# Kernel tuning notes

Hardware: AMD Instinct MI355X
Metric: run time of the kernel (lower is better)

The kernel has to match this reference:

```python
import jax, jax.numpy as jnp
import numpy as np

N_HEAD = 16
N_FEAT = 1024
D_K = N_FEAT // N_HEAD
BATCH = 8
SEQ = 1024
LN_EPS = 1e-5
MIN_VAL = float(np.finfo(np.float32).min)


def setup_inputs() -> dict:
    key = jax.random.key(0)
    ks = jax.random.split(key, 8)
    s = 0.02  # small init scale for weights to keep activations sane
    return {
        "x": jax.random.normal(ks[0], (BATCH, SEQ, N_FEAT), jnp.float32),
        "pos_k": jax.random.normal(ks[1], (SEQ, SEQ, D_K), jnp.float32) * s,
        "mask": jnp.ones((BATCH, SEQ, SEQ), jnp.int32),
        "ln_scale": jnp.ones((N_FEAT,), jnp.float32),
        "ln_bias": jnp.zeros((N_FEAT,), jnp.float32),
        "wq": jax.random.normal(ks[2], (N_FEAT, N_FEAT), jnp.float32) * s,
        "bq": jnp.zeros((N_FEAT,), jnp.float32),
        "wk": jax.random.normal(ks[3], (N_FEAT, N_FEAT), jnp.float32) * s,
        "bk": jnp.zeros((N_FEAT,), jnp.float32),
        "wv": jax.random.normal(ks[4], (N_FEAT, N_FEAT), jnp.float32) * s,
        "bv": jnp.zeros((N_FEAT,), jnp.float32),
        "wo": jax.random.normal(ks[5], (N_FEAT, N_FEAT), jnp.float32) * s,
        "bo": jnp.zeros((N_FEAT,), jnp.float32),
    }


def reference(x, pos_k, mask, ln_scale, ln_bias, wq, bq, wk, bk, wv, bv, wo, bo):
    b, t, f = x.shape
    h, d = N_HEAD, D_K
    # LayerNorm over feature dim
    mu = jnp.mean(x, axis=-1, keepdims=True)
    var = jnp.mean((x - mu) ** 2, axis=-1, keepdims=True)
    xn = (x - mu) / jnp.sqrt(var + LN_EPS) * ln_scale + ln_bias
    # QKV projections (torch Linear: y = x @ W^T + b), split heads -> (b, h, t, d)
    q = (xn @ wq.T + bq).reshape(b, t, h, d).transpose(0, 2, 1, 3)
    k = (xn @ wk.T + bk).reshape(b, t, h, d).transpose(0, 2, 1, 3)
    v = (xn @ wv.T + bv).reshape(b, t, h, d).transpose(0, 2, 1, 3)
    # content score A and relative-position score B
    A = jnp.einsum("bhtd,bhsd->bhts", q, k)
    B = jnp.einsum("bhtd,tsd->bhts", q, pos_k)
    scores = (A + B) / jnp.sqrt(jnp.asarray(d, scores_dtype := x.dtype))
    m = (mask[:, None, :, :] == 0)  # (b, 1, t, s) broadcast over heads
    scores = jnp.where(m, MIN_VAL, scores)
    attn = jax.nn.softmax(scores, axis=-1)
    attn = jnp.where(m, 0.0, attn)
    out = jnp.einsum("bhts,bhsd->bhtd", attn, v)
    out = out.transpose(0, 2, 1, 3).reshape(b, t, h * d)
    return out @ wo.T + bo
```

## Files before the change

### kernel.cpp

```cpp
#include <hip/hip_runtime.h>
#include <hip/hip_bf16.h>

typedef unsigned short ushort_t;
typedef short short8 __attribute__((ext_vector_type(8)));
typedef unsigned short ushort8 __attribute__((ext_vector_type(8)));
typedef unsigned short ushortx4 __attribute__((ext_vector_type(4)));
typedef float fx4 __attribute__((ext_vector_type(4)));
typedef int ix4 __attribute__((ext_vector_type(4)));

#define MFMA(a, b, c) __builtin_amdgcn_mfma_f32_16x16x32_bf16((a), (b), (c), 0, 0, 0)

#define QSCALE 0.18033688011112042f

__device__ __forceinline__ ushort_t f2bf(float f) {
  __hip_bfloat16 h = __float2bfloat16(f);
  return *(ushort_t*)&h;
}
__device__ __forceinline__ float bf2f(ushort_t h) {
  union { unsigned u; float f; } c; c.u = ((unsigned)h) << 16;
  return c.f;
}
__device__ __forceinline__ void gload16(const ushort_t* g, ushort_t* l) {
  __builtin_amdgcn_global_load_lds((const __attribute__((address_space(1))) void*)g,
                                   (__attribute__((address_space(3))) void*)l, 16, 0, 0);
}
template <int R>
__device__ __forceinline__ float fp8sel(unsigned u) {
  return __builtin_amdgcn_cvt_f32_fp8((int)u, R);
}
__device__ __forceinline__ fx4 fp8x4(unsigned u) {
  fx4 r;
  r[0] = fp8sel<0>(u); r[1] = fp8sel<1>(u); r[2] = fp8sel<2>(u); r[3] = fp8sel<3>(u);
  return r;
}

__global__ __launch_bounds__(256) void cvt4_kernel(const float* __restrict__ s0,
                                                   const float* __restrict__ s1,
                                                   const float* __restrict__ s2,
                                                   const float* __restrict__ s3,
                                                   ushort_t* __restrict__ d0,
                                                   ushort_t* __restrict__ d1,
                                                   ushort_t* __restrict__ d2,
                                                   ushort_t* __restrict__ d3) {
  int bi = blockIdx.x;
  const float* src = (bi < 1024) ? s0 : (bi < 2048) ? s1 : (bi < 3072) ? s2 : s3;
  ushort_t* dst = (bi < 1024) ? d0 : (bi < 2048) ? d1 : (bi < 3072) ? d2 : d3;
  int i = (bi & 1023) * 256 + threadIdx.x;
  fx4 v = *(const fx4*)&src[(size_t)i * 4];
  ushortx4 o;
#pragma unroll
  for (int j = 0; j < 4; ++j) o[j] = f2bf(v[j]);
  *(ushortx4*)&dst[(size_t)i * 4] = o;
}

__global__ __launch_bounds__(256) void ln_kernel(const float* __restrict__ x,
                                                 const float* __restrict__ sc,
                                                 const float* __restrict__ bi,
                                                 ushort_t* __restrict__ xn) {
  __shared__ float red[8];
  int row = blockIdx.x, tid = threadIdx.x;
  const float* xr = x + (size_t)row * 1024;
  fx4 v = *(const fx4*)&xr[tid * 4];
  float s = v[0] + v[1] + v[2] + v[3];
  float s2 = v[0] * v[0] + v[1] * v[1] + v[2] * v[2] + v[3] * v[3];
#pragma unroll
  for (int m = 32; m >= 1; m >>= 1) {
    s += __shfl_xor(s, m);
    s2 += __shfl_xor(s2, m);
  }
  int wave = tid >> 6;
  if ((tid & 63) == 0) { red[wave * 2] = s; red[wave * 2 + 1] = s2; }
  __syncthreads();
  s = red[0] + red[2] + red[4] + red[6];
  s2 = red[1] + red[3] + red[5] + red[7];
  float mu = s * (1.f / 1024.f);
  float var = s2 * (1.f / 1024.f) - mu * mu;
  float rs = rsqrtf(var + 1e-5f);
  fx4 scv = *(const fx4*)&sc[tid * 4];
  fx4 biv = *(const fx4*)&bi[tid * 4];
  ushortx4 o;
#pragma unroll
  for (int j = 0; j < 4; ++j) o[j] = f2bf((v[j] - mu) * rs * scv[j] + biv[j]);
  *(ushortx4*)&xn[(size_t)row * 1024 + tid * 4] = o;
}

__global__ __launch_bounds__(256) void maskpack_kernel(const int* __restrict__ mask,
                                                       unsigned* __restrict__ bits) {
  __shared__ unsigned char nib[256];
  int row = blockIdx.x, tid = threadIdx.x;
  ix4 m = *(const ix4*)&mask[(size_t)row * 1024 + tid * 4];
  nib[tid] = (unsigned char)((m[0] != 0 ? 1 : 0) | (m[1] != 0 ? 2 : 0) |
                             (m[2] != 0 ? 4 : 0) | (m[3] != 0 ? 8 : 0));
  __syncthreads();
  if (tid < 32) {
    unsigned w = 0;
#pragma unroll
    for (int j = 0; j < 8; ++j) w |= ((unsigned)nib[tid * 8 + j]) << (j * 4);
    bits[(size_t)row * 32 + tid] = w;
  }
}

template <int F32OUT>
__global__ __launch_bounds__(256) void gemm_bt(const ushort_t* __restrict__ A,
                                               const ushort_t* __restrict__ B,
                                               const float* __restrict__ b0,
                                               const float* __restrict__ b1,
                                               const float* __restrict__ b2, void* C,
                                               int M, int N, int K, float os0, float os1) {
  __shared__ ushort_t lA[4096];
  __shared__ ushort_t lB[4096];
  int bm = blockIdx.y * 128, bn = blockIdx.x * 128;
  int tid = threadIdx.x;
  int wave = tid >> 6, lane = tid & 63;
  int wm = (wave >> 1) * 64, wn = (wave & 1) * 64;
  int l15 = lane & 15, lg = lane >> 4;
  int r0 = tid >> 2, c0 = (tid & 3) * 8;
  int g1 = 256 + tid, r1 = g1 >> 2, c1 = (g1 & 3) * 8;
  int lb0 = (wave * 64) * 8;
  int lb1 = (256 + wave * 64) * 8;
  fx4 acc[4][4] = {};
  for (int k0 = 0; k0 < K; k0 += 32) {
    __syncthreads();
    gload16(&A[(size_t)(bm + r0) * K + k0 + c0], &lA[lb0]);
    gload16(&A[(size_t)(bm + r1) * K + k0 + c1], &lA[lb1]);
    gload16(&B[(size_t)(bn + r0) * K + k0 + c0], &lB[lb0]);
    gload16(&B[(size_t)(bn + r1) * K + k0 + c1], &lB[lb1]);
    __syncthreads();
    short8 af[4], bf[4];
#pragma unroll
    for (int i = 0; i < 4; ++i) af[i] = *(const short8*)&lA[(wm + i * 16 + l15) * 32 + lg * 8];
#pragma unroll
    for (int i = 0; i < 4; ++i) bf[i] = *(const short8*)&lB[(wn + i * 16 + l15) * 32 + lg * 8];
#pragma unroll
    for (int i = 0; i < 4; ++i)
#pragma unroll
      for (int j = 0; j < 4; ++j) acc[i][j] = MFMA(af[i], bf[j], acc[i][j]);
  }
#pragma unroll
  for (int j = 0; j < 4; ++j) {
    int n = bn + wn + j * 16 + l15;
    const float* bp = (n < 1024) ? b0 : (n < 2048) ? b1 : b2;
    float bv = bp[n & 1023];
    float sc = (n < 1024) ? os0 : os1;
#pragma unroll
    for (int i = 0; i < 4; ++i) {
      int mr = bm + wm + i * 16 + lg * 4;
#pragma unroll
      for (int r = 0; r < 4; ++r) {
        float val = (acc[i][j][r] + bv) * sc;
        if (F32OUT)
          ((float*)C)[(size_t)(mr + r) * N + n] = val;
        else
          ((ushort_t*)C)[(size_t)(mr + r) * N + n] = f2bf(val);
      }
    }
  }
}

__device__ __forceinline__ void loadset(const float* base, int c, fx4* r) {
  const float* p = base + (size_t)c * 1024;
  r[0] = *(const fx4*)p;
  r[1] = *(const fx4*)(p + 4);
  r[2] = *(const fx4*)(p + 32);
  r[3] = *(const fx4*)(p + 36);
}
__device__ __forceinline__ void cvtset(const fx4* r, short8& f0, short8& f1) {
#pragma unroll
  for (int j = 0; j < 4; ++j) {
    f0[j] = (short)f2bf(r[0][j]); f0[j + 4] = (short)f2bf(r[1][j]);
    f1[j] = (short)f2bf(r[2][j]); f1[j + 4] = (short)f2bf(r[3][j]);
  }
}

__global__ __launch_bounds__(512, 4) void ball_kernel(const ushort_t* __restrict__ qkv,
                                                      const float* __restrict__ pos_k,
                                                      unsigned char* __restrict__ B8) {
  __shared__ ushort_t lq[128 * 64];
  int t = blockIdx.y, sx = blockIdx.x;
  int tid = threadIdx.x, wave = tid >> 6, lane = tid & 63, l15 = lane & 15, lg = lane >> 4;
  const float* pk = pos_k + (size_t)t * 65536;
  int sw = sx * 512 + wave * 64;
  const float* base = pk + (size_t)(sw + l15) * 64 + lg * 8;

  fx4 raw[4][4];
#pragma unroll
  for (int c = 0; c < 4; ++c) loadset(base, c, raw[c]);

#pragma unroll
  for (int it = 0; it < 2; ++it) {
    int u = tid + it * 512;
    int row = u >> 3, cu = u & 7;
    ushort8 vv = *(const ushort8*)&qkv[((size_t)((row >> 4) * 1024 + t)) * 3072 + (row & 15) * 64 + cu * 8];
    *(ushort8*)&lq[(row * 128 + ((cu * 16) ^ ((row & 7) << 4))) >> 1] = vv;
  }
  __syncthreads();

  short8 af0[4], af1[4];
#pragma unroll
  for (int c = 0; c < 4; ++c) cvtset(raw[c], af0[c], af1[c]);

#pragma unroll
  for (int j = 0; j < 8; ++j) {
    int row_ = j * 16 + l15;
    int cb_ = (row_ & 7) << 4;
    short8 q0 = *(const short8*)&lq[(row_ * 128 + ((lg * 16) ^ cb_)) >> 1];
    short8 q1 = *(const short8*)&lq[(row_ * 128 + ((64 + lg * 16) ^ cb_)) >> 1];
    fx4 z = {};
    size_t rb = ((size_t)row_ << 20) + (size_t)t * 1024 + (size_t)sw;
#pragma unroll
    for (int c = 0; c < 4; ++c) {
      fx4 a = MFMA(af0[c], q0, z);
      a = MFMA(af1[c], q1, a);
      int u = __builtin_amdgcn_cvt_pk_fp8_f32(a[0], a[1], 0, false);
      u = __builtin_amdgcn_cvt_pk_fp8_f32(a[2], a[3], u, true);
      *(unsigned*)&B8[rb + c * 16 + lg * 4] = (unsigned)u;
    }
  }
}

__global__ __launch_bounds__(256) void attn_kernel(const ushort_t* __restrict__ qkv,
                                                   const unsigned char* __restrict__ B8,
                                                   const unsigned* __restrict__ mbits,
                                                   ushort_t* __restrict__ out) {
  __shared__ ushort_t lK[64][72];
  __shared__ ushort_t lVt[64][72];
  __shared__ ushort_t lP[4][2][16][72];
  int bh = blockIdx.y, b = bh >> 4, h = bh & 15;
  int t0 = blockIdx.x * 128;
  int tid = threadIdx.x, wave = tid >> 6, lane = tid & 63, l15 = lane & 15, lg = lane >> 4;
  int twA = t0 + wave * 16, twB = twA + 64;
  short8 qfA[2], qfB[2];
#pragma unroll
  for (int ks = 0; ks < 2; ++ks) {
    qfA[ks] = *(const short8*)&qkv[((size_t)(b * 1024 + twA + l15)) * 3072 + h * 64 + ks * 32 + lg * 8];
    qfB[ks] = *(const short8*)&qkv[((size_t)(b * 1024 + twB + l15)) * 3072 + h * 64 + ks * 32 + lg * 8];
  }
  fx4 oA[4] = {}, oB[4] = {};
  float lsumA = 0.f, lsumB = 0.f;
  const unsigned* mrowA = &mbits[((size_t)b * 1024 + twA + l15) * 32];
  const unsigned* mrowB = &mbits[((size_t)b * 1024 + twB + l15) * 32];
  size_t ballA = ((size_t)bh * 1024 + twA + l15) * 1024;
  size_t ballB = ((size_t)bh * 1024 + twB + l15) * 1024;

  int rs = tid >> 3, c8g = tid & 7, c8 = c8g * 8;
  const ushort_t* kbase = &qkv[((size_t)(b * 1024) + rs) * 3072 + 1024 + h * 64 + c8];
  const ushort_t* vbase = &qkv[((size_t)(b * 1024) + rs) * 3072 + 2048 + h * 64 + c8];
  ushort8 kr0 = *(const ushort8*)(kbase);
  ushort8 kr1 = *(const ushort8*)(kbase + 32 * 3072);
  ushort8 vr0 = *(const ushort8*)(vbase);
  ushort8 vr1 = *(const ushort8*)(vbase + 32 * 3072);
  int vs0 = (rs + 8 * c8g) & 63;
  int vs1 = (rs + 32 + 8 * c8g) & 63;

  unsigned n8A[4], n8B[4];
#pragma unroll
  for (int mf = 0; mf < 4; ++mf) {
    n8A[mf] = *(const unsigned*)&B8[ballA + mf * 16 + lg * 4];
    n8B[mf] = *(const unsigned*)&B8[ballB + mf * 16 + lg * 4];
  }
  uint2 nmA = *(const uint2*)&mrowA[0];
  uint2 nmB = *(const uint2*)&mrowB[0];

  for (int s0 = 0; s0 < 1024; s0 += 64) {
    __syncthreads();
    *(ushort8*)&lK[rs][c8] = kr0;
    *(ushort8*)&lK[rs + 32][c8] = kr1;
#pragma unroll
    for (int j = 0; j < 8; ++j) {
      lVt[c8 + j][vs0] = vr0[j];
      lVt[c8 + j][vs1] = vr1[j];
    }
    __syncthreads();
    if (s0 + 64 < 1024) {
      size_t off = (size_t)(s0 + 64) * 3072;
      kr0 = *(const ushort8*)(kbase + off);
      kr1 = *(const ushort8*)(kbase + off + 32 * 3072);
      vr0 = *(const ushort8*)(vbase + off);
      vr1 = *(const ushort8*)(vbase + off + 32 * 3072);
    }
    __builtin_amdgcn_sched_barrier(0);
    unsigned long long wbA = ((unsigned long long)nmA.y << 32) | nmA.x;
    unsigned long long wbB = ((unsigned long long)nmB.y << 32) | nmB.x;
    float pA[16], pB[16];
#pragma unroll
    for (int mf = 0; mf < 4; ++mf) {
      short8 kf0 = *(const short8*)&lK[mf * 16 + l15][lg * 8];
      short8 kf1 = *(const short8*)&lK[mf * 16 + l15][32 + lg * 8];
      fx4 cA = {}, cB = {};
      cA = MFMA(kf0, qfA[0], cA);
      cA = MFMA(kf1, qfA[1], cA);
      cB = MFMA(kf0, qfB[0], cB);
      cB = MFMA(kf1, qfB[1], cB);
      fx4 dA = fp8x4(n8A[mf]);
      fx4 dB = fp8x4(n8B[mf]);
#pragma unroll
      for (int r = 0; r < 4; ++r) {
        pA[mf * 4 + r] = exp2f(cA[r] + dA[r]);
        pB[mf * 4 + r] = exp2f(cB[r] + dB[r]);
      }
    }
    if (!__all((wbA == ~0ull) && (wbB == ~0ull))) {
#pragma unroll
      for (int i = 0; i < 16; ++i) {
        int sl = (i >> 2) * 16 + lg * 4 + (i & 3);
        if (!((wbA >> sl) & 1ull)) pA[i] = 0.f;
        if (!((wbB >> sl) & 1ull)) pB[i] = 0.f;
      }
    }
    if (s0 + 64 < 1024) {
#pragma unroll
      for (int mf = 0; mf < 4; ++mf) {
        n8A[mf] = *(const unsigned*)&B8[ballA + s0 + 64 + mf * 16 + lg * 4];
        n8B[mf] = *(const unsigned*)&B8[ballB + s0 + 64 + mf * 16 + lg * 4];
      }
      nmA = *(const uint2*)&mrowA[(s0 + 64) >> 5];
      nmB = *(const uint2*)&mrowB[(s0 + 64) >> 5];
    }
    __builtin_amdgcn_sched_barrier(0);
    float psA = 0.f, psB = 0.f;
#pragma unroll
    for (int i = 0; i < 16; ++i) { psA += pA[i]; psB += pB[i]; }
    lsumA += psA;
    lsumB += psB;
#pragma unroll
    for (int mf = 0; mf < 4; ++mf) {
      ushortx4 pk4A, pk4B;
#pragma unroll
      for (int r = 0; r < 4; ++r) { pk4A[r] = f2bf(pA[mf * 4 + r]); pk4B[r] = f2bf(pB[mf * 4 + r]); }
      *(ushortx4*)&lP[wave][0][l15][mf * 16 + lg * 4] = pk4A;
      *(ushortx4*)&lP[wave][1][l15][mf * 16 + lg * 4] = pk4B;
    }
#pragma unroll
    for (int ks = 0; ks < 2; ++ks) {
      short8 pfA = *(const short8*)&lP[wave][0][l15][ks * 32 + lg * 8];
      short8 pfB = *(const short8*)&lP[wave][1][l15][ks * 32 + lg * 8];
#pragma unroll
      for (int nf = 0; nf < 4; ++nf) {
        int d_ = nf * 16 + l15;
        int sb_ = (ks * 32 + lg * 8 + 8 * (d_ >> 3)) & 63;
        short8 vf = *(const short8*)&lVt[d_][sb_];
        oA[nf] = MFMA(pfA, vf, oA[nf]);
        oB[nf] = MFMA(pfB, vf, oB[nf]);
      }
    }
  }
  lsumA += __shfl_xor(lsumA, 16);
  lsumA += __shfl_xor(lsumA, 32);
  lsumB += __shfl_xor(lsumB, 16);
  lsumB += __shfl_xor(lsumB, 32);
  float rlA = (lsumA > 0.f) ? 1.f / lsumA : 0.f;
  float rlB = (lsumB > 0.f) ? 1.f / lsumB : 0.f;
  float rwA[4], rwB[4];
#pragma unroll
  for (int r = 0; r < 4; ++r) {
    rwA[r] = __shfl(rlA, lg * 4 + r);
    rwB[r] = __shfl(rlB, lg * 4 + r);
  }
#pragma unroll
  for (int nf = 0; nf < 4; ++nf)
#pragma unroll
    for (int r = 0; r < 4; ++r) {
      out[((size_t)(b * 1024 + twA + lg * 4 + r)) * 1024 + h * 64 + nf * 16 + l15] =
          f2bf(oA[nf][r] * rwA[r]);
      out[((size_t)(b * 1024 + twB + lg * 4 + r)) * 1024 + h * 64 + nf * 16 + l15] =
          f2bf(oB[nf][r] * rwB[r]);
    }
}

extern "C" void kernel_launch(void* const* d_in, const int* in_sizes, int n_in, void* d_out,
                              int out_size, void* d_ws, size_t ws_size, hipStream_t stream) {
  (void)in_sizes; (void)n_in; (void)out_size; (void)ws_size;
  const float* x = (const float*)d_in[0];
  const float* pos_k = (const float*)d_in[1];
  const int* mask = (const int*)d_in[2];
  const float* ln_scale = (const float*)d_in[3];
  const float* ln_bias = (const float*)d_in[4];
  const float* wq = (const float*)d_in[5];
  const float* bq = (const float*)d_in[6];
  const float* wk = (const float*)d_in[7];
  const float* bk = (const float*)d_in[8];
  const float* wv = (const float*)d_in[9];
  const float* bv = (const float*)d_in[10];
  const float* wo = (const float*)d_in[11];
  const float* bo = (const float*)d_in[12];
  float* out = (float*)d_out;
  char* ws = (char*)d_ws;
  const size_t MB = 1ull << 20;
  ushort_t* xn = (ushort_t*)(ws + 0 * MB);
  ushort_t* qkv = (ushort_t*)(ws + 16 * MB);
  ushort_t* ao = (ushort_t*)(ws + 64 * MB);
  ushort_t* wqb = (ushort_t*)(ws + 80 * MB);
  ushort_t* wkb = (ushort_t*)(ws + 82 * MB);
  ushort_t* wvb = (ushort_t*)(ws + 84 * MB);
  ushort_t* wob = (ushort_t*)(ws + 86 * MB);
  unsigned char* ball8 = (unsigned char*)(ws + 88 * MB);
  unsigned* mbits = (unsigned*)(ws + 0 * MB);

  cvt4_kernel<<<4096, 256, 0, stream>>>(wq, wk, wv, wo, wqb, wkb, wvb, wob);
  ln_kernel<<<8192, 256, 0, stream>>>(x, ln_scale, ln_bias, xn);
  gemm_bt<0><<<dim3(24, 64), 256, 0, stream>>>(xn, wqb, bq, bk, bv, qkv, 8192, 3072, 1024,
                                               QSCALE, 1.f);
  maskpack_kernel<<<8192, 256, 0, stream>>>(mask, mbits);
  ball_kernel<<<dim3(2, 1024), 512, 0, stream>>>(qkv, pos_k, ball8);
  attn_kernel<<<dim3(8, 128), 256, 0, stream>>>(qkv, ball8, mbits, ao);
  gemm_bt<1><<<dim3(8, 64), 256, 0, stream>>>(ao, wob, bo, bo, bo, out, 8192, 1024, 1024,
                                              1.f, 1.f);
}
```

Measured before the change: 354.5 us.

## Merge prep kernels into one launch and double-buffer pos_k loads in ball kernel

The weight-conversion, LayerNorm and mask-packing kernels are combined into one prep kernel dispatched by block index, and the mask bits move to a separate workspace offset so they no longer alias xn. The ball kernel now has each block handle all 1024 s positions for one t. Each wave covers 128 columns in two halves and prefetches the second pos_k chunk while the first half's MFMAs run. This cuts launch count and hides pos_k load latency, but halves the ball grid and raises register pressure from the prefetch.

```diff
diff --git a/kernel.cpp b/kernel.cpp
--- a/kernel.cpp
+++ b/kernel.cpp
@@ -34,69 +34,69 @@
   return r;
 }
 
-__global__ __launch_bounds__(256) void cvt4_kernel(const float* __restrict__ s0,
-                                                   const float* __restrict__ s1,
-                                                   const float* __restrict__ s2,
-                                                   const float* __restrict__ s3,
-                                                   ushort_t* __restrict__ d0,
-                                                   ushort_t* __restrict__ d1,
-                                                   ushort_t* __restrict__ d2,
-                                                   ushort_t* __restrict__ d3) {
-  int bi = blockIdx.x;
-  const float* src = (bi < 1024) ? s0 : (bi < 2048) ? s1 : (bi < 3072) ? s2 : s3;
-  ushort_t* dst = (bi < 1024) ? d0 : (bi < 2048) ? d1 : (bi < 3072) ? d2 : d3;
-  int i = (bi & 1023) * 256 + threadIdx.x;
-  fx4 v = *(const fx4*)&src[(size_t)i * 4];
-  ushortx4 o;
-#pragma unroll
-  for (int j = 0; j < 4; ++j) o[j] = f2bf(v[j]);
-  *(ushortx4*)&dst[(size_t)i * 4] = o;
-}
-
-__global__ __launch_bounds__(256) void ln_kernel(const float* __restrict__ x,
-                                                 const float* __restrict__ sc,
-                                                 const float* __restrict__ bi,
-                                                 ushort_t* __restrict__ xn) {
+__global__ __launch_bounds__(256) void prep_kernel(const float* __restrict__ wq,
+                                                   const float* __restrict__ wk,
+                                                   const float* __restrict__ wv,
+                                                   const float* __restrict__ wo,
+                                                   ushort_t* __restrict__ wqb,
+                                                   ushort_t* __restrict__ wkb,
+                                                   ushort_t* __restrict__ wvb,
+                                                   ushort_t* __restrict__ wob,
+                                                   const float* __restrict__ x,
+                                                   const float* __restrict__ sc,
+                                                   const float* __restrict__ bi,
+                                                   ushort_t* __restrict__ xn,
+                                                   const int* __restrict__ mask,
+                                                   unsigned* __restrict__ bits) {
   __shared__ float red[8];
-  int row = blockIdx.x, tid = threadIdx.x;
-  const float* xr = x + (size_t)row * 1024;
-  fx4 v = *(const fx4*)&xr[tid * 4];
-  float s = v[0] + v[1] + v[2] + v[3];
-  float s2 = v[0] * v[0] + v[1] * v[1] + v[2] * v[2] + v[3] * v[3];
-#pragma unroll
-  for (int m = 32; m >= 1; m >>= 1) {
-    s += __shfl_xor(s, m);
-    s2 += __shfl_xor(s2, m);
-  }
-  int wave = tid >> 6;
-  if ((tid & 63) == 0) { red[wave * 2] = s; red[wave * 2 + 1] = s2; }
-  __syncthreads();
-  s = red[0] + red[2] + red[4] + red[6];
-  s2 = red[1] + red[3] + red[5] + red[7];
-  float mu = s * (1.f / 1024.f);
-  float var = s2 * (1.f / 1024.f) - mu * mu;
-  float rs = rsqrtf(var + 1e-5f);
-  fx4 scv = *(const fx4*)&sc[tid * 4];
-  fx4 biv = *(const fx4*)&bi[tid * 4];
-  ushortx4 o;
-#pragma unroll
-  for (int j = 0; j < 4; ++j) o[j] = f2bf((v[j] - mu) * rs * scv[j] + biv[j]);
-  *(ushortx4*)&xn[(size_t)row * 1024 + tid * 4] = o;
-}
-
-__global__ __launch_bounds__(256) void maskpack_kernel(const int* __restrict__ mask,
-                                                       unsigned* __restrict__ bits) {
   __shared__ unsigned char nib[256];
-  int row = blockIdx.x, tid = threadIdx.x;
-  ix4 m = *(const ix4*)&mask[(size_t)row * 1024 + tid * 4];
-  nib[tid] = (unsigned char)((m[0] != 0 ? 1 : 0) | (m[1] != 0 ? 2 : 0) |
-                             (m[2] != 0 ? 4 : 0) | (m[3] != 0 ? 8 : 0));
-  __syncthreads();
-  if (tid < 32) {
-    unsigned w = 0;
-#pragma unroll
-    for (int j = 0; j < 8; ++j) w |= ((unsigned)nib[tid * 8 + j]) << (j * 4);
-    bits[(size_t)row * 32 + tid] = w;
+  int bid = blockIdx.x, tid = threadIdx.x;
+  if (bid < 4096) {
+    const float* src = (bid < 1024) ? wq : (bid < 2048) ? wk : (bid < 3072) ? wv : wo;
+    ushort_t* dst = (bid < 1024) ? wqb : (bid < 2048) ? wkb : (bid < 3072) ? wvb : wob;
+    int i = (bid & 1023) * 256 + tid;
+    fx4 v = *(const fx4*)&src[(size_t)i * 4];
+    ushortx4 o;
+#pragma unroll
+    for (int j = 0; j < 4; ++j) o[j] = f2bf(v[j]);
+    *(ushortx4*)&dst[(size_t)i * 4] = o;
+  } else if (bid < 12288) {
+    int row = bid - 4096;
+    const float* xr = x + (size_t)row * 1024;
+    fx4 v = *(const fx4*)&xr[tid * 4];
+    float s = v[0] + v[1] + v[2] + v[3];
+    float s2 = v[0] * v[0] + v[1] * v[1] + v[2] * v[2] + v[3] * v[3];
+#pragma unroll
+    for (int m = 32; m >= 1; m >>= 1) {
+      s += __shfl_xor(s, m);
+      s2 += __shfl_xor(s2, m);
+    }
+    int wave = tid >> 6;
+    if ((tid & 63) == 0) { red[wave * 2] = s; red[wave * 2 + 1] = s2; }
+    __syncthreads();
+    s = red[0] + red[2] + red[4] + red[6];
+    s2 = red[1] + red[3] + red[5] + red[7];
+    float mu = s * (1.f / 1024.f);
+    float var = s2 * (1.f / 1024.f) - mu * mu;
+    float rs = rsqrtf(var + 1e-5f);
+    fx4 scv = *(const fx4*)&sc[tid * 4];
+    fx4 biv = *(const fx4*)&bi[tid * 4];
+    ushortx4 o;
+#pragma unroll
+    for (int j = 0; j < 4; ++j) o[j] = f2bf((v[j] - mu) * rs * scv[j] + biv[j]);
+    *(ushortx4*)&xn[(size_t)row * 1024 + tid * 4] = o;
+  } else {
+    int row = bid - 12288;
+    ix4 m = *(const ix4*)&mask[(size_t)row * 1024 + tid * 4];
+    nib[tid] = (unsigned char)((m[0] != 0 ? 1 : 0) | (m[1] != 0 ? 2 : 0) |
+                               (m[2] != 0 ? 4 : 0) | (m[3] != 0 ? 8 : 0));
+    __syncthreads();
+    if (tid < 32) {
+      unsigned w = 0;
+#pragma unroll
+      for (int j = 0; j < 8; ++j) w |= ((unsigned)nib[tid * 8 + j]) << (j * 4);
+      bits[(size_t)row * 32 + tid] = w;
+    }
   }
 }
 
@@ -176,10 +176,10 @@
                                                       const float* __restrict__ pos_k,
                                                       unsigned char* __restrict__ B8) {
   __shared__ ushort_t lq[128 * 64];
-  int t = blockIdx.y, sx = blockIdx.x;
+  int t = blockIdx.x;
   int tid = threadIdx.x, wave = tid >> 6, lane = tid & 63, l15 = lane & 15, lg = lane >> 4;
   const float* pk = pos_k + (size_t)t * 65536;
-  int sw = sx * 512 + wave * 64;
+  int sw = wave * 128;
   const float* base = pk + (size_t)(sw + l15) * 64 + lg * 8;
 
   fx4 raw[4][4];
@@ -200,20 +200,33 @@
   for (int c = 0; c < 4; ++c) cvtset(raw[c], af0[c], af1[c]);
 
 #pragma unroll
-  for (int j = 0; j < 8; ++j) {
-    int row_ = j * 16 + l15;
-    int cb_ = (row_ & 7) << 4;
-    short8 q0 = *(const short8*)&lq[(row_ * 128 + ((lg * 16) ^ cb_)) >> 1];
-    short8 q1 = *(const short8*)&lq[(row_ * 128 + ((64 + lg * 16) ^ cb_)) >> 1];
-    fx4 z = {};
-    size_t rb = ((size_t)row_ << 20) + (size_t)t * 1024 + (size_t)sw;
-#pragma unroll
-    for (int c = 0; c < 4; ++c) {
-      fx4 a = MFMA(af0[c], q0, z);
-      a = MFMA(af1[c], q1, a);
-      int u = __builtin_amdgcn_cvt_pk_fp8_f32(a[0], a[1], 0, false);
-      u = __builtin_amdgcn_cvt_pk_fp8_f32(a[2], a[3], u, true);
-      *(unsigned*)&B8[rb + c * 16 + lg * 4] = (unsigned)u;
+  for (int g = 0; g < 2; ++g) {
+    if (g == 0) {
+#pragma unroll
+      for (int c = 0; c < 4; ++c) loadset(base, 4 + c, raw[c]);
+    }
+    __builtin_amdgcn_sched_barrier(0);
+#pragma unroll
+    for (int j = 0; j < 8; ++j) {
+      int row_ = j * 16 + l15;
+      int cb_ = (row_ & 7) << 4;
+      short8 q0 = *(const short8*)&lq[(row_ * 128 + ((lg * 16) ^ cb_)) >> 1];
+      short8 q1 = *(const short8*)&lq[(row_ * 128 + ((64 + lg * 16) ^ cb_)) >> 1];
+      fx4 z = {};
+      size_t rb = ((size_t)row_ << 20) + (size_t)t * 1024 + (size_t)(sw + g * 64);
+#pragma unroll
+      for (int c = 0; c < 4; ++c) {
+        fx4 a = MFMA(af0[c], q0, z);
+        a = MFMA(af1[c], q1, a);
+        int u = __builtin_amdgcn_cvt_pk_fp8_f32(a[0], a[1], 0, false);
+        u = __builtin_amdgcn_cvt_pk_fp8_f32(a[2], a[3], u, true);
+        *(unsigned*)&B8[rb + c * 16 + lg * 4] = (unsigned)u;
+      }
+    }
+    __builtin_amdgcn_sched_barrier(0);
+    if (g == 0) {
+#pragma unroll
+      for (int c = 0; c < 4; ++c) cvtset(raw[c], af0[c], af1[c]);
     }
   }
 }
@@ -394,14 +407,13 @@
   ushort_t* wvb = (ushort_t*)(ws + 84 * MB);
   ushort_t* wob = (ushort_t*)(ws + 86 * MB);
   unsigned char* ball8 = (unsigned char*)(ws + 88 * MB);
-  unsigned* mbits = (unsigned*)(ws + 0 * MB);
-
-  cvt4_kernel<<<4096, 256, 0, stream>>>(wq, wk, wv, wo, wqb, wkb, wvb, wob);
-  ln_kernel<<<8192, 256, 0, stream>>>(x, ln_scale, ln_bias, xn);
+  unsigned* mbits = (unsigned*)(ws + 216 * MB);
+
+  prep_kernel<<<20480, 256, 0, stream>>>(wq, wk, wv, wo, wqb, wkb, wvb, wob, x, ln_scale,
+                                         ln_bias, xn, mask, mbits);
   gemm_bt<0><<<dim3(24, 64), 256, 0, stream>>>(xn, wqb, bq, bk, bv, qkv, 8192, 3072, 1024,
                                                QSCALE, 1.f);
-  maskpack_kernel<<<8192, 256, 0, stream>>>(mask, mbits);
-  ball_kernel<<<dim3(2, 1024), 512, 0, stream>>>(qkv, pos_k, ball8);
+  ball_kernel<<<1024, 512, 0, stream>>>(qkv, pos_k, ball8);
   attn_kernel<<<dim3(8, 128), 256, 0, stream>>>(qkv, ball8, mbits, ao);
   gemm_bt<1><<<dim3(8, 64), 256, 0, stream>>>(ao, wob, bo, bo, bo, out, 8192, 1024, 1024,
                                               1.f, 1.f);
```

Measured after the change: 387.5 us. 9.3% more time.
